# Kernel optimization log

Measured on AMD Instinct MI355X. Metric: run time of the kernel, lower is better.

## Reference

```python
import jax, jax.numpy as jnp
import numpy as np

NH, HS, K = 32, 2048, 16
HD = HS // NH
B, L = 4, 2048
EPS = 1e-6

def _ln(x, gamma, beta):
    mu = x.mean(-1, keepdims=True)
    var = x.var(-1, keepdims=True)  # ddof=0 == torch unbiased=False
    return gamma * ((x - mu) / jnp.sqrt(var + EPS)) + beta

def _ln_fused_l2_bwd(x, target, gamma, beta):
    D = x.shape[-1]
    mu = x.mean(-1, keepdims=True)
    std = jnp.sqrt(x.var(-1, keepdims=True) + EPS)
    xh = (x - mu) / std
    gxh = (gamma * xh + beta - target) * gamma
    return (D * gxh - gxh.sum(-1, keepdims=True) - xh * (gxh * xh).sum(-1, keepdims=True)) / (D * std)

def setup_inputs() -> dict:
    key = jax.random.key(0)
    ks = jax.random.split(key, 8)
    s = 0.02
    return {
        'hidden_states': jax.random.normal(ks[0], (B, L, HS), jnp.float32),
        'position_ids': jnp.tile(jnp.arange(L, dtype=jnp.int32)[None], (B, 1)),
        'q_w': jax.random.normal(ks[1], (HS, HS), jnp.float32) * s,
        'k_w': jax.random.normal(ks[2], (HS, HS), jnp.float32) * s,
        'v_w': jax.random.normal(ks[3], (HS, HS), jnp.float32) * s,
        'o_w': jax.random.normal(ks[4], (HS, HS), jnp.float32) * s,
        'W1': jax.random.normal(ks[5], (NH, HD, HD), jnp.float32) * s,
        'b1': jnp.zeros((NH, 1, HD), jnp.float32),
        'ttt_norm_weight': jnp.ones((NH, HD), jnp.float32),
        'ttt_norm_bias': jnp.zeros((NH, HD), jnp.float32),
        'ttt_lr_weight': jax.random.normal(ks[6], (NH, 1, HS), jnp.float32) * s,
        'ttt_lr_bias': jnp.zeros((NH, 1), jnp.float32),
        'learnable_token_idx': jnp.zeros((K,), jnp.float32),
        'post_norm_weight': jnp.ones((HS,), jnp.float32),
        'post_norm_bias': jnp.zeros((HS,), jnp.float32),
    }

def _forward(hidden_states, q_w, k_w, v_w, o_w, W1, b1, ttt_norm_weight,
             ttt_norm_bias, ttt_lr_weight, ttt_lr_bias, learnable_token_idx,
             post_norm_weight, post_norm_bias):
    Bb, Ll, _ = hidden_states.shape
    NM = Ll // K

    def proj_heads(w):
        return (hidden_states @ w.T).reshape(Bb, Ll, NH, HD).transpose(0, 2, 1, 3)

    XQ = proj_heads(q_w).reshape(Bb, NH, NM, K, HD)
    XK = proj_heads(k_w).reshape(Bb, NH, NM, K, HD)
    XV = proj_heads(v_w).reshape(Bb, NH, NM, K, HD)
    X = hidden_states.reshape(Bb, NM, K, HS)

    # eta: learned per-token lr gate, [B,nh,NM,K,K]
    ttt_lr = jnp.einsum('bnkc,hdc->bhnkd', X, ttt_lr_weight) + ttt_lr_bias.reshape(1, NH, 1, 1, 1)
    ttt_lr_eta = jax.nn.sigmoid(ttt_lr).transpose(0, 1, 2, 4, 3) / HD  # ttt_base_lr = 1.0
    token_idx = jnp.clip(1.0 / jnp.arange(1, K + 1, dtype=jnp.float32) + learnable_token_idx, 0.0, None)
    eta = token_idx.reshape(1, 1, 1, K, 1) * ttt_lr_eta

    ln_w = ttt_norm_weight.reshape(NH, 1, HD)
    ln_b = ttt_norm_bias.reshape(NH, 1, HD)

    def step(carry, x):
        W1_s, b1_s = carry                 # [B,nh,hd,hd], [B,nh,1,hd]
        xq, xk, xv, eta_mb = x             # [B,nh,K,hd], eta_mb [B,nh,K,K]
        Z1 = xk @ W1_s + b1_s
        grad = _ln_fused_l2_bwd(Z1, xv - xk, ln_w, ln_b)
        Attn1 = jnp.tril(xq @ xk.swapaxes(-1, -2))
        b1_bar = b1_s - jnp.tril(eta_mb) @ grad
        Z1_bar = xq @ W1_s - (eta_mb * Attn1) @ grad + b1_bar
        last_eta = eta_mb[:, :, -1, :, None]  # [B,nh,K,1]
        W1_new = W1_s - (last_eta * xk).swapaxes(-1, -2) @ grad
        b1_new = b1_s - jnp.sum(last_eta * grad, axis=-2, keepdims=True)
        out = xq + _ln(Z1_bar, ln_w, ln_b)
        return (W1_new, b1_new), out

    init = (jnp.tile(W1[None], (Bb, 1, 1, 1)), jnp.tile(b1[None], (Bb, 1, 1, 1)))
    xs = (XQ.transpose(2, 0, 1, 3, 4), XK.transpose(2, 0, 1, 3, 4),
          XV.transpose(2, 0, 1, 3, 4), eta.transpose(2, 0, 1, 3, 4))
    _, ys = jax.lax.scan(step, init, xs)          # [NM,B,nh,K,hd]
    out = ys.transpose(1, 0, 3, 2, 4).reshape(Bb, Ll, HS)
    out = _ln(out, post_norm_weight, post_norm_bias)  # post_norm (eps 1e-6)
    return out @ o_w.T

def reference(hidden_states, position_ids, q_w, k_w, v_w, o_w, W1, b1,
              ttt_norm_weight, ttt_norm_bias, ttt_lr_weight, ttt_lr_bias,
              learnable_token_idx, post_norm_weight, post_norm_bias):
    del position_ids  # unused in the shown forward (rope never applied)
    return _forward(hidden_states, q_w, k_w, v_w, o_w, W1, b1, ttt_norm_weight,
                    ttt_norm_bias, ttt_lr_weight, ttt_lr_bias, learnable_token_idx,
                    post_norm_weight, post_norm_bias)
```

## Files before the change

kernel.cpp:

```cpp
#include <hip/hip_runtime.h>

typedef unsigned short u16;
typedef unsigned int u32;
typedef __bf16 bf16_t;
typedef bf16_t bf16x8 __attribute__((ext_vector_type(8)));
typedef float f32x4 __attribute__((ext_vector_type(4)));
typedef u16 u16x8 __attribute__((ext_vector_type(8)));

#define B_   4
#define L_   2048
#define HS_  2048
#define NH_  32
#define HD_  64
#define KK_  16
#define NM_  128
#define M_   (B_*L_)

__device__ __forceinline__ u16 f2bf(float f) {
  unsigned u = __float_as_uint(f);
  u += 0x7FFFu + ((u >> 16) & 1u);
  return (u16)(u >> 16);
}
__device__ __forceinline__ float bf2f(u16 u) {
  return __uint_as_float(((unsigned)u) << 16);
}
__device__ __forceinline__ f32x4 vshfl_xor(f32x4 v, int m) {
  f32x4 r;
  r[0] = __shfl_xor(v[0], m, 64); r[1] = __shfl_xor(v[1], m, 64);
  r[2] = __shfl_xor(v[2], m, 64); r[3] = __shfl_xor(v[3], m, 64);
  return r;
}

__global__ __launch_bounds__(256) void cast_f32_bf16(const float* __restrict__ in,
                                                     u16* __restrict__ out, int n) {
  int i = (blockIdx.x * 256 + threadIdx.x) * 8;
  if (i >= n) return;
  float4 a = *(const float4*)(in + i);
  float4 b = *(const float4*)(in + i + 4);
  u16x8 o;
  o[0]=f2bf(a.x); o[1]=f2bf(a.y); o[2]=f2bf(a.z); o[3]=f2bf(a.w);
  o[4]=f2bf(b.x); o[5]=f2bf(b.y); o[6]=f2bf(b.z); o[7]=f2bf(b.w);
  *(u16x8*)(out + i) = o;
}

#define BM 128
#define BN 128
#define BK 32
#define LDT 40

template <bool BF16OUT>
__global__ __launch_bounds__(256) void gemm_nt(const u16* __restrict__ A,
                                               const u16* __restrict__ Bt,
                                               void* __restrict__ Cv,
                                               int M, int N, int K) {
  __shared__ u16 As[BM * LDT];
  __shared__ u16 Bs[BN * LDT];
  int tid  = threadIdx.x;
  int lane = tid & 63, wave = tid >> 6;
  int quad = lane >> 4, l16 = lane & 15;
  int bM = blockIdx.x * BM, bN = blockIdx.y * BN;
  int wM = (wave >> 1) * 64, wN = (wave & 1) * 64;
  int r0 = tid >> 2, c0 = (tid & 3) * 8;
  const u16* Ap = A + (size_t)bM * K;
  const u16* Bp = Bt + (size_t)bN * K;
  f32x4 acc[4][4] = {};
  u16x8 pa0 = *(const u16x8*)(Ap + (size_t)r0 * K + c0);
  u16x8 pa1 = *(const u16x8*)(Ap + (size_t)(r0 + 64) * K + c0);
  u16x8 pb0 = *(const u16x8*)(Bp + (size_t)r0 * K + c0);
  u16x8 pb1 = *(const u16x8*)(Bp + (size_t)(r0 + 64) * K + c0);
  int nk = K / BK;
  for (int kt = 0; kt < nk; ++kt) {
    *(u16x8*)&As[r0 * LDT + c0]        = pa0;
    *(u16x8*)&As[(r0 + 64) * LDT + c0] = pa1;
    *(u16x8*)&Bs[r0 * LDT + c0]        = pb0;
    *(u16x8*)&Bs[(r0 + 64) * LDT + c0] = pb1;
    __syncthreads();
    if (kt + 1 < nk) {
      int k0 = (kt + 1) * BK + c0;
      pa0 = *(const u16x8*)(Ap + (size_t)r0 * K + k0);
      pa1 = *(const u16x8*)(Ap + (size_t)(r0 + 64) * K + k0);
      pb0 = *(const u16x8*)(Bp + (size_t)r0 * K + k0);
      pb1 = *(const u16x8*)(Bp + (size_t)(r0 + 64) * K + k0);
    }
    bf16x8 af[4], bfr[4];
#pragma unroll
    for (int i = 0; i < 4; ++i) {
      u16x8 t = *(const u16x8*)&As[(wM + i * 16 + l16) * LDT + quad * 8];
      af[i] = __builtin_bit_cast(bf16x8, t);
    }
#pragma unroll
    for (int j = 0; j < 4; ++j) {
      u16x8 t = *(const u16x8*)&Bs[(wN + j * 16 + l16) * LDT + quad * 8];
      bfr[j] = __builtin_bit_cast(bf16x8, t);
    }
#pragma unroll
    for (int i = 0; i < 4; ++i) {
#pragma unroll
      for (int j = 0; j < 4; ++j)
        acc[i][j] = __builtin_amdgcn_mfma_f32_16x16x32_bf16(af[i], bfr[j], acc[i][j], 0, 0, 0);
    }
    __syncthreads();
  }
#pragma unroll
  for (int i = 0; i < 4; ++i) {
#pragma unroll
    for (int j = 0; j < 4; ++j) {
      int row = bM + wM + i * 16 + quad * 4;
      int col = bN + wN + j * 16 + l16;
      if (BF16OUT) {
        u16* cp = (u16*)Cv + (size_t)row * N + col;
#pragma unroll
        for (int r = 0; r < 4; ++r) cp[(size_t)r * N] = f2bf(acc[i][j][r]);
      } else {
        float* cp = (float*)Cv + (size_t)row * N + col;
#pragma unroll
        for (int r = 0; r < 4; ++r) cp[(size_t)r * N] = acc[i][j][r];
      }
    }
  }
}

__global__ __launch_bounds__(256) void sig_kernel(const u16* __restrict__ hsb,
                                                  const u16* __restrict__ lrwb,
                                                  const float* __restrict__ lrb,
                                                  float* __restrict__ Sig) {
  __shared__ u16 Bs[32 * LDT];
  int tid = threadIdx.x;
  int lane = tid & 63, wave = tid >> 6;
  int quad = lane >> 4, l16 = lane & 15;
  int m0 = blockIdx.x * 64 + wave * 16;
  f32x4 acc0 = {}, acc1 = {};
  for (int kt = 0; kt < HS_ / BK; ++kt) {
    int k0 = kt * BK;
    if (tid < 128) {
      int r = tid >> 2, c8 = (tid & 3) * 8;
      *(u16x8*)&Bs[r * LDT + c8] = *(const u16x8*)(lrwb + (size_t)r * HS_ + k0 + c8);
    }
    __syncthreads();
    u16x8 ta = *(const u16x8*)(hsb + (size_t)(m0 + l16) * HS_ + k0 + quad * 8);
    u16x8 t0 = *(const u16x8*)&Bs[l16 * LDT + quad * 8];
    u16x8 t1 = *(const u16x8*)&Bs[(16 + l16) * LDT + quad * 8];
    bf16x8 af  = __builtin_bit_cast(bf16x8, ta);
    bf16x8 bf0 = __builtin_bit_cast(bf16x8, t0);
    bf16x8 bf1 = __builtin_bit_cast(bf16x8, t1);
    acc0 = __builtin_amdgcn_mfma_f32_16x16x32_bf16(af, bf0, acc0, 0, 0, 0);
    acc1 = __builtin_amdgcn_mfma_f32_16x16x32_bf16(af, bf1, acc1, 0, 0, 0);
    __syncthreads();
  }
#pragma unroll
  for (int j = 0; j < 2; ++j) {
    f32x4 a = j ? acc1 : acc0;
    int h = j * 16 + l16;
    float bias = lrb[h];
#pragma unroll
    for (int r = 0; r < 4; ++r) {
      int m = m0 + quad * 4 + r;
      float v = a[r] + bias;
      float s = (1.f / (1.f + expf(-v))) * (1.f / 64.f);
      Sig[(size_t)m * NH_ + h] = s;
    }
  }
}

__global__ __launch_bounds__(256) void ttt_scan_mfma(
    const u16* __restrict__ XQ, const u16* __restrict__ XK, const u16* __restrict__ XV,
    const float* __restrict__ Sig, const float* __restrict__ W1_0, const float* __restrict__ b1_0,
    const float* __restrict__ lnw, const float* __restrict__ lnb, const float* __restrict__ lti,
    float* __restrict__ Y) {
  __shared__ u16 xkq[32 * 72];
  __shared__ u16 W1t[64 * 72];
  __shared__ u16 gradT[64 * 40];
  __shared__ u16 coefA[16 * 40];
  __shared__ u16 xkT[64 * 40];
  __shared__ float diff[16 * 68];
  __shared__ float red1[128], red2[128], red3[128];
  __shared__ float sig_s[16];

  int tid = threadIdx.x, wave = tid >> 6, lane = tid & 63;
  int quad = lane >> 4, l16 = lane & 15;
  int bh = blockIdx.x, b = bh >> 5, h = bh & 31;
  int dcol = wave * 16 + l16;

  {
    u32* p = (u32*)gradT; for (int i = tid; i < 1280; i += 256) p[i] = 0;
    u32* q = (u32*)coefA; for (int i = tid; i < 320;  i += 256) q[i] = 0;
    u32* s = (u32*)xkT;   for (int i = tid; i < 1280; i += 256) s[i] = 0;
  }

  f32x4 master[4];
  const float* wsrc = W1_0 + (size_t)h * 4096 + (size_t)dcol * 64;
#pragma unroll
  for (int m = 0; m < 4; ++m)
#pragma unroll
    for (int r = 0; r < 4; ++r) master[m][r] = wsrc[m * 16 + quad * 4 + r];
#pragma unroll
  for (int m = 0; m < 4; ++m)
#pragma unroll
    for (int r = 0; r < 4; ++r)
      W1t[(m * 16 + quad * 4 + r) * 72 + dcol] = f2bf(master[m][r]);

  float b1_reg = b1_0[h * 64 + dcol];
  float gamma_r = lnw[h * 64 + dcol], beta_r = lnb[h * 64 + dcol];
  f32x4 tok4;
#pragma unroll
  for (int r = 0; r < 4; ++r) {
    int kk = quad * 4 + r;
    tok4[r] = fmaxf(1.0f / (float)(kk + 1) + lti[kk], 0.0f);
  }
  float tok15 = fmaxf(1.0f / 16.0f + lti[15], 0.0f);

  int lrow = (tid < 128) ? (tid >> 3) : ((tid - 128) >> 3);
  int lc8  = (tid & 7) * 8;
  size_t rowstep = (size_t)HS_;
  size_t gb0 = ((size_t)(b * L_ + lrow)) * HS_ + h * HD_ + lc8;

  u16x8 rq, rv, rk;
  float rsig = 0.f;
  {
    size_t g = gb0;
    if (tid < 128) { rq = *(const u16x8*)(XQ + g); rv = *(const u16x8*)(XV + g); rk = *(const u16x8*)(XK + g); }
    else           { rk = *(const u16x8*)(XK + g); }
    if (tid < 16) rsig = Sig[(size_t)(b * L_ + tid) * NH_ + h];
  }
  __syncthreads();

  for (int n = 0; n < NM_; ++n) {
    if (tid < 128) {
      *(u16x8*)&xkq[(16 + lrow) * 72 + lc8] = rq;
      float4 d0, d1;
      d0.x = bf2f(rv[0]) - bf2f(rk[0]); d0.y = bf2f(rv[1]) - bf2f(rk[1]);
      d0.z = bf2f(rv[2]) - bf2f(rk[2]); d0.w = bf2f(rv[3]) - bf2f(rk[3]);
      d1.x = bf2f(rv[4]) - bf2f(rk[4]); d1.y = bf2f(rv[5]) - bf2f(rk[5]);
      d1.z = bf2f(rv[6]) - bf2f(rk[6]); d1.w = bf2f(rv[7]) - bf2f(rk[7]);
      *(float4*)&diff[lrow * 68 + lc8]     = d0;
      *(float4*)&diff[lrow * 68 + lc8 + 4] = d1;
    } else {
      *(u16x8*)&xkq[lrow * 72 + lc8] = rk;
#pragma unroll
      for (int i = 0; i < 8; ++i)
        xkT[(lc8 + i) * 40 + lrow] = f2bf(-tok15 * bf2f(rk[i]));
    }
    if (tid < 16) sig_s[tid] = rsig;
    __syncthreads();

    if (n + 1 < NM_) {
      size_t g = gb0 + (size_t)(n + 1) * KK_ * rowstep;
      if (tid < 128) { rq = *(const u16x8*)(XQ + g); rv = *(const u16x8*)(XV + g); rk = *(const u16x8*)(XK + g); }
      else           { rk = *(const u16x8*)(XK + g); }
      if (tid < 16) rsig = Sig[(size_t)(b * L_ + (n + 1) * KK_ + tid) * NH_ + h];
    }

    bf16x8 fxk[2], fxq[2], fw[2];
#pragma unroll
    for (int kc = 0; kc < 2; ++kc) {
      fxk[kc] = __builtin_bit_cast(bf16x8, *(const u16x8*)&xkq[l16 * 72 + kc * 32 + quad * 8]);
      fxq[kc] = __builtin_bit_cast(bf16x8, *(const u16x8*)&xkq[(16 + l16) * 72 + kc * 32 + quad * 8]);
      fw[kc]  = __builtin_bit_cast(bf16x8, *(const u16x8*)&W1t[(wave * 16 + l16) * 72 + kc * 32 + quad * 8]);
    }
    f32x4 z1 = {}, zq = {};
#pragma unroll
    for (int kc = 0; kc < 2; ++kc) {
      z1 = __builtin_amdgcn_mfma_f32_16x16x32_bf16(fxk[kc], fw[kc], z1, 0, 0, 0);
      zq = __builtin_amdgcn_mfma_f32_16x16x32_bf16(fxq[kc], fw[kc], zq, 0, 0, 0);
    }
    if (wave == 0) {
      f32x4 at = {};
#pragma unroll
      for (int kc = 0; kc < 2; ++kc)
        at = __builtin_amdgcn_mfma_f32_16x16x32_bf16(fxq[kc], fxk[kc], at, 0, 0, 0);
#pragma unroll
      for (int r = 0; r < 4; ++r) {
        int kk = quad * 4 + r;
        float c = (l16 <= kk) ? tok4[r] * (1.0f + at[r]) : 0.0f;
        coefA[kk * 40 + l16] = f2bf(-c);
      }
    }
#pragma unroll
    for (int r = 0; r < 4; ++r) z1[r] += b1_reg;

    {
      f32x4 s1 = z1, s2 = z1 * z1;
#pragma unroll
      for (int m = 1; m <= 8; m <<= 1) { s1 = s1 + vshfl_xor(s1, m); s2 = s2 + vshfl_xor(s2, m); }
      if (l16 == 0) {
#pragma unroll
        for (int r = 0; r < 4; ++r) {
          red1[quad * 32 + r * 8 + wave]     = s1[r];
          red1[quad * 32 + r * 8 + 4 + wave] = s2[r];
        }
      }
    }
    __syncthreads();
    f32x4 mu, rstd;
#pragma unroll
    for (int r = 0; r < 4; ++r) {
      f32x4 a = *(const f32x4*)&red1[quad * 32 + r * 8];
      f32x4 c = *(const f32x4*)&red1[quad * 32 + r * 8 + 4];
      float S = a[0] + a[1] + a[2] + a[3];
      float SS = c[0] + c[1] + c[2] + c[3];
      mu[r] = S * (1.0f / 64.0f);
      float var = SS * (1.0f / 64.0f) - mu[r] * mu[r];
      rstd[r] = 1.0f / sqrtf(var + 1e-6f);
    }
    f32x4 xh, gxh;
#pragma unroll
    for (int r = 0; r < 4; ++r) {
      float dd = diff[(quad * 4 + r) * 68 + dcol];
      xh[r] = (z1[r] - mu[r]) * rstd[r];
      gxh[r] = (gamma_r * xh[r] + beta_r - dd) * gamma_r;
    }
    {
      f32x4 s1 = gxh, s2 = gxh * xh;
#pragma unroll
      for (int m = 1; m <= 8; m <<= 1) { s1 = s1 + vshfl_xor(s1, m); s2 = s2 + vshfl_xor(s2, m); }
      if (l16 == 0) {
#pragma unroll
        for (int r = 0; r < 4; ++r) {
          red2[quad * 32 + r * 8 + wave]     = s1[r];
          red2[quad * 32 + r * 8 + 4 + wave] = s2[r];
        }
      }
    }
    __syncthreads();
    f32x4 grad;
#pragma unroll
    for (int r = 0; r < 4; ++r) {
      f32x4 a = *(const f32x4*)&red2[quad * 32 + r * 8];
      f32x4 c = *(const f32x4*)&red2[quad * 32 + r * 8 + 4];
      float S1v = a[0] + a[1] + a[2] + a[3];
      float S2v = c[0] + c[1] + c[2] + c[3];
      grad[r] = (64.0f * gxh[r] - S1v - xh[r] * S2v) * (rstd[r] * (1.0f / 64.0f));
    }
#pragma unroll
    for (int r = 0; r < 4; ++r) {
      float sk = sig_s[quad * 4 + r];
      gradT[dcol * 40 + quad * 4 + r] = f2bf(sk * grad[r]);
    }
    __syncthreads();

    bf16x8 fA = __builtin_bit_cast(bf16x8, *(const u16x8*)&coefA[l16 * 40 + quad * 8]);
    bf16x8 fG = __builtin_bit_cast(bf16x8, *(const u16x8*)&gradT[(wave * 16 + l16) * 40 + quad * 8]);
    f32x4 zb = __builtin_amdgcn_mfma_f32_16x16x32_bf16(fA, fG, zq, 0, 0, 0);
#pragma unroll
    for (int r = 0; r < 4; ++r) zb[r] += b1_reg;
    {
      bf16x8 fX = __builtin_bit_cast(bf16x8, *(const u16x8*)&xkT[(wave * 16 + l16) * 40 + quad * 8]);
#pragma unroll
      for (int m = 0; m < 4; ++m) {
        bf16x8 fGm = __builtin_bit_cast(bf16x8, *(const u16x8*)&gradT[(m * 16 + l16) * 40 + quad * 8]);
        master[m] = __builtin_amdgcn_mfma_f32_16x16x32_bf16(fGm, fX, master[m], 0, 0, 0);
      }
      float bs = 0.f;
#pragma unroll
      for (int j = 0; j < 8; ++j) bs += (float)fG[j];
      bs += __shfl_xor(bs, 16, 64);
      bs += __shfl_xor(bs, 32, 64);
      b1_reg -= tok15 * bs;
    }
    {
      f32x4 s1 = zb, s2 = zb * zb;
#pragma unroll
      for (int m = 1; m <= 8; m <<= 1) { s1 = s1 + vshfl_xor(s1, m); s2 = s2 + vshfl_xor(s2, m); }
      if (l16 == 0) {
#pragma unroll
        for (int r = 0; r < 4; ++r) {
          red3[quad * 32 + r * 8 + wave]     = s1[r];
          red3[quad * 32 + r * 8 + 4 + wave] = s2[r];
        }
      }
    }
    __syncthreads();
#pragma unroll
    for (int r = 0; r < 4; ++r) {
      f32x4 a = *(const f32x4*)&red3[quad * 32 + r * 8];
      f32x4 c = *(const f32x4*)&red3[quad * 32 + r * 8 + 4];
      float S = a[0] + a[1] + a[2] + a[3];
      float SS = c[0] + c[1] + c[2] + c[3];
      float mu2 = S * (1.0f / 64.0f);
      float var2 = SS * (1.0f / 64.0f) - mu2 * mu2;
      float rstd2 = 1.0f / sqrtf(var2 + 1e-6f);
      float xq_pass = bf2f(xkq[(16 + quad * 4 + r) * 72 + dcol]);
      float yv = xq_pass + gamma_r * ((zb[r] - mu2) * rstd2) + beta_r;
      Y[((size_t)(b * L_ + n * KK_ + quad * 4 + r)) * HS_ + h * HD_ + dcol] = yv;
    }
#pragma unroll
    for (int m = 0; m < 4; ++m)
#pragma unroll
      for (int r = 0; r < 4; ++r)
        W1t[(m * 16 + quad * 4 + r) * 72 + dcol] = f2bf(master[m][r]);
    __syncthreads();
  }
}

__global__ __launch_bounds__(256) void postnorm(const float* __restrict__ Yin,
                                                const float* __restrict__ w,
                                                const float* __restrict__ bb,
                                                u16* __restrict__ Yn) {
  __shared__ float red[8];
  int row = blockIdx.x, tid = threadIdx.x;
  const float* x = Yin + (size_t)row * HS_ + tid * 8;
  float4 v0 = *(const float4*)(x);
  float4 v1 = *(const float4*)(x + 4);
  float s  = v0.x + v0.y + v0.z + v0.w + v1.x + v1.y + v1.z + v1.w;
  float ss = v0.x*v0.x + v0.y*v0.y + v0.z*v0.z + v0.w*v0.w
           + v1.x*v1.x + v1.y*v1.y + v1.z*v1.z + v1.w*v1.w;
#pragma unroll
  for (int m = 32; m > 0; m >>= 1) { s += __shfl_xor(s, m, 64); ss += __shfl_xor(ss, m, 64); }
  int wave = tid >> 6, lane = tid & 63;
  if (lane == 0) { red[wave] = s; red[4 + wave] = ss; }
  __syncthreads();
  float S  = red[0] + red[1] + red[2] + red[3];
  float SS = red[4] + red[5] + red[6] + red[7];
  float mu = S * (1.f / 2048.f);
  float var = SS * (1.f / 2048.f) - mu * mu;
  float rstd = 1.f / sqrtf(var + 1e-6f);
  const float* wp = w + tid * 8;
  const float* bp = bb + tid * 8;
  float vals[8] = {v0.x, v0.y, v0.z, v0.w, v1.x, v1.y, v1.z, v1.w};
  u16x8 o;
#pragma unroll
  for (int t = 0; t < 8; ++t) o[t] = f2bf(wp[t] * ((vals[t] - mu) * rstd) + bp[t]);
  *(u16x8*)(Yn + (size_t)row * HS_ + tid * 8) = o;
}

extern "C" void kernel_launch(void* const* d_in, const int* in_sizes, int n_in,
                              void* d_out, int out_size, void* d_ws, size_t ws_size,
                              hipStream_t stream) {
  (void)in_sizes; (void)n_in; (void)out_size; (void)ws_size;
  const float* hidden = (const float*)d_in[0];
  const float* q_w = (const float*)d_in[2];
  const float* k_w = (const float*)d_in[3];
  const float* v_w = (const float*)d_in[4];
  const float* o_w = (const float*)d_in[5];
  const float* W1  = (const float*)d_in[6];
  const float* b1i = (const float*)d_in[7];
  const float* lnw = (const float*)d_in[8];
  const float* lnb = (const float*)d_in[9];
  const float* lrw = (const float*)d_in[10];
  const float* lrb = (const float*)d_in[11];
  const float* lti = (const float*)d_in[12];
  const float* pnw = (const float*)d_in[13];
  const float* pnb = (const float*)d_in[14];
  float* out = (float*)d_out;

  char* w = (char*)d_ws;
  u16* hsb  = (u16*)w;  w += (size_t)16777216 * 2;
  u16* wb   = (u16*)w;  w += (size_t)4194304 * 2;
  u16* lrwb = (u16*)w;  w += (size_t)65536 * 2;
  u16* XQb  = (u16*)w;  w += (size_t)16777216 * 2;
  u16* XKb  = (u16*)w;  w += (size_t)16777216 * 2;
  u16* XVb  = (u16*)w;  w += (size_t)16777216 * 2;
  float* Sg = (float*)w; w += (size_t)M_ * NH_ * 4;
  u16* Yn = hsb;

  cast_f32_bf16<<<8192, 256, 0, stream>>>(hidden, hsb, 16777216);
  cast_f32_bf16<<<32, 256, 0, stream>>>(lrw, lrwb, 65536);

  sig_kernel<<<128, 256, 0, stream>>>(hsb, lrwb, lrb, Sg);

  dim3 gg(M_ / BM, HS_ / BN);
  cast_f32_bf16<<<2048, 256, 0, stream>>>(q_w, wb, 4194304);
  gemm_nt<true><<<gg, 256, 0, stream>>>(hsb, wb, XQb, M_, HS_, HS_);
  cast_f32_bf16<<<2048, 256, 0, stream>>>(k_w, wb, 4194304);
  gemm_nt<true><<<gg, 256, 0, stream>>>(hsb, wb, XKb, M_, HS_, HS_);
  cast_f32_bf16<<<2048, 256, 0, stream>>>(v_w, wb, 4194304);
  gemm_nt<true><<<gg, 256, 0, stream>>>(hsb, wb, XVb, M_, HS_, HS_);

  ttt_scan_mfma<<<128, 256, 0, stream>>>(XQb, XKb, XVb, Sg, W1, b1i, lnw, lnb, lti, out);

  postnorm<<<8192, 256, 0, stream>>>(out, pnw, pnb, Yn);

  cast_f32_bf16<<<2048, 256, 0, stream>>>(o_w, wb, 4194304);
  gemm_nt<false><<<gg, 256, 0, stream>>>(Yn, wb, out, M_, HS_, HS_);
}
```

Baseline: 1.017 ms.

## Run TTT scan with one wave per head, removing block barriers

```diff
diff --git a/kernel.cpp b/kernel.cpp
--- a/kernel.cpp
+++ b/kernel.cpp
@@ -162,45 +162,55 @@
   }
 }
 
-__global__ __launch_bounds__(256) void ttt_scan_mfma(
+__global__ __launch_bounds__(64, 1) void ttt_scan_wave(
     const u16* __restrict__ XQ, const u16* __restrict__ XK, const u16* __restrict__ XV,
     const float* __restrict__ Sig, const float* __restrict__ W1_0, const float* __restrict__ b1_0,
     const float* __restrict__ lnw, const float* __restrict__ lnb, const float* __restrict__ lti,
     float* __restrict__ Y) {
-  __shared__ u16 xkq[32 * 72];
   __shared__ u16 W1t[64 * 72];
   __shared__ u16 gradT[64 * 40];
   __shared__ u16 coefA[16 * 40];
   __shared__ u16 xkT[64 * 40];
-  __shared__ float diff[16 * 68];
-  __shared__ float red1[128], red2[128], red3[128];
-  __shared__ float sig_s[16];
-
-  int tid = threadIdx.x, wave = tid >> 6, lane = tid & 63;
+  __shared__ float diffS[16 * 68];
+  __shared__ float xqF[16 * 68];
+
+  int lane = threadIdx.x;
   int quad = lane >> 4, l16 = lane & 15;
   int bh = blockIdx.x, b = bh >> 5, h = bh & 31;
-  int dcol = wave * 16 + l16;
 
   {
-    u32* p = (u32*)gradT; for (int i = tid; i < 1280; i += 256) p[i] = 0;
-    u32* q = (u32*)coefA; for (int i = tid; i < 320;  i += 256) q[i] = 0;
-    u32* s = (u32*)xkT;   for (int i = tid; i < 1280; i += 256) s[i] = 0;
-  }
-
-  f32x4 master[4];
-  const float* wsrc = W1_0 + (size_t)h * 4096 + (size_t)dcol * 64;
-#pragma unroll
-  for (int m = 0; m < 4; ++m)
-#pragma unroll
-    for (int r = 0; r < 4; ++r) master[m][r] = wsrc[m * 16 + quad * 4 + r];
-#pragma unroll
-  for (int m = 0; m < 4; ++m)
-#pragma unroll
-    for (int r = 0; r < 4; ++r)
-      W1t[(m * 16 + quad * 4 + r) * 72 + dcol] = f2bf(master[m][r]);
-
-  float b1_reg = b1_0[h * 64 + dcol];
-  float gamma_r = lnw[h * 64 + dcol], beta_r = lnb[h * 64 + dcol];
+    u32* p = (u32*)gradT; for (int i = lane; i < 1280; i += 64) p[i] = 0;
+    u32* q = (u32*)coefA; for (int i = lane; i < 320;  i += 64) q[i] = 0;
+    u32* s = (u32*)xkT;   for (int i = lane; i < 1280; i += 64) s[i] = 0;
+  }
+
+  f32x4 master[4][4];
+  {
+    const float* wsrc = W1_0 + (size_t)h * 4096;
+#pragma unroll
+    for (int c = 0; c < 4; ++c) {
+      const float* wc = wsrc + (size_t)(c * 16 + l16) * 64 + quad * 4;
+#pragma unroll
+      for (int a = 0; a < 4; ++a)
+#pragma unroll
+        for (int r = 0; r < 4; ++r) master[a][c][r] = wc[a * 16 + r];
+    }
+  }
+#pragma unroll
+  for (int a = 0; a < 4; ++a)
+#pragma unroll
+    for (int c = 0; c < 4; ++c)
+#pragma unroll
+      for (int r = 0; r < 4; ++r)
+        W1t[(a * 16 + quad * 4 + r) * 72 + c * 16 + l16] = f2bf(master[a][c][r]);
+
+  f32x4 b1r, gam, bet;
+#pragma unroll
+  for (int c = 0; c < 4; ++c) {
+    b1r[c] = b1_0[h * 64 + c * 16 + l16];
+    gam[c] = lnw[h * 64 + c * 16 + l16];
+    bet[c] = lnb[h * 64 + c * 16 + l16];
+  }
   f32x4 tok4;
 #pragma unroll
   for (int r = 0; r < 4; ++r) {
@@ -209,186 +219,192 @@
   }
   float tok15 = fmaxf(1.0f / 16.0f + lti[15], 0.0f);
 
-  int lrow = (tid < 128) ? (tid >> 3) : ((tid - 128) >> 3);
-  int lc8  = (tid & 7) * 8;
-  size_t rowstep = (size_t)HS_;
-  size_t gb0 = ((size_t)(b * L_ + lrow)) * HS_ + h * HD_ + lc8;
-
-  u16x8 rq, rv, rk;
-  float rsig = 0.f;
-  {
-    size_t g = gb0;
-    if (tid < 128) { rq = *(const u16x8*)(XQ + g); rv = *(const u16x8*)(XV + g); rk = *(const u16x8*)(XK + g); }
-    else           { rk = *(const u16x8*)(XK + g); }
-    if (tid < 16) rsig = Sig[(size_t)(b * L_ + tid) * NH_ + h];
-  }
-  __syncthreads();
+  size_t gb  = ((size_t)(b * L_ + l16)) * HS_ + h * HD_ + quad * 8;
+  size_t sgb = (size_t)(b * L_ + l16) * NH_ + h;
+
+  u16x8 cxk[2], cxq[2], cxv[2];
+  float csig;
+#pragma unroll
+  for (int kc = 0; kc < 2; ++kc) {
+    cxk[kc] = *(const u16x8*)(XK + gb + kc * 32);
+    cxq[kc] = *(const u16x8*)(XQ + gb + kc * 32);
+    cxv[kc] = *(const u16x8*)(XV + gb + kc * 32);
+  }
+  csig = Sig[sgb];
 
   for (int n = 0; n < NM_; ++n) {
-    if (tid < 128) {
-      *(u16x8*)&xkq[(16 + lrow) * 72 + lc8] = rq;
-      float4 d0, d1;
-      d0.x = bf2f(rv[0]) - bf2f(rk[0]); d0.y = bf2f(rv[1]) - bf2f(rk[1]);
-      d0.z = bf2f(rv[2]) - bf2f(rk[2]); d0.w = bf2f(rv[3]) - bf2f(rk[3]);
-      d1.x = bf2f(rv[4]) - bf2f(rk[4]); d1.y = bf2f(rv[5]) - bf2f(rk[5]);
-      d1.z = bf2f(rv[6]) - bf2f(rk[6]); d1.w = bf2f(rv[7]) - bf2f(rk[7]);
-      *(float4*)&diff[lrow * 68 + lc8]     = d0;
-      *(float4*)&diff[lrow * 68 + lc8 + 4] = d1;
-    } else {
-      *(u16x8*)&xkq[lrow * 72 + lc8] = rk;
-#pragma unroll
-      for (int i = 0; i < 8; ++i)
-        xkT[(lc8 + i) * 40 + lrow] = f2bf(-tok15 * bf2f(rk[i]));
-    }
-    if (tid < 16) sig_s[tid] = rsig;
-    __syncthreads();
+    bf16x8 fw[4][2];
+#pragma unroll
+    for (int cb = 0; cb < 4; ++cb)
+#pragma unroll
+      for (int kc = 0; kc < 2; ++kc)
+        fw[cb][kc] = __builtin_bit_cast(bf16x8,
+            *(const u16x8*)&W1t[(cb * 16 + l16) * 72 + kc * 32 + quad * 8]);
+
+#pragma unroll
+    for (int kc = 0; kc < 2; ++kc) {
+      float dv[8], qv[8];
+#pragma unroll
+      for (int j = 0; j < 8; ++j) {
+        dv[j] = bf2f(cxv[kc][j]) - bf2f(cxk[kc][j]);
+        qv[j] = bf2f(cxq[kc][j]);
+      }
+      float4 d0 = {dv[0], dv[1], dv[2], dv[3]}, d1 = {dv[4], dv[5], dv[6], dv[7]};
+      float4 q0 = {qv[0], qv[1], qv[2], qv[3]}, q1 = {qv[4], qv[5], qv[6], qv[7]};
+      *(float4*)&diffS[l16 * 68 + kc * 32 + quad * 8]     = d0;
+      *(float4*)&diffS[l16 * 68 + kc * 32 + quad * 8 + 4] = d1;
+      *(float4*)&xqF[l16 * 68 + kc * 32 + quad * 8]       = q0;
+      *(float4*)&xqF[l16 * 68 + kc * 32 + quad * 8 + 4]   = q1;
+#pragma unroll
+      for (int j = 0; j < 8; ++j)
+        xkT[(kc * 32 + quad * 8 + j) * 40 + l16] = f2bf(-tok15 * bf2f(cxk[kc][j]));
+    }
+    f32x4 ssig;
+#pragma unroll
+    for (int r = 0; r < 4; ++r) ssig[r] = __shfl(csig, quad * 4 + r, 64);
+
+    bf16x8 fxk[2], fxq[2];
+#pragma unroll
+    for (int kc = 0; kc < 2; ++kc) {
+      fxk[kc] = __builtin_bit_cast(bf16x8, cxk[kc]);
+      fxq[kc] = __builtin_bit_cast(bf16x8, cxq[kc]);
+    }
 
     if (n + 1 < NM_) {
-      size_t g = gb0 + (size_t)(n + 1) * KK_ * rowstep;
-      if (tid < 128) { rq = *(const u16x8*)(XQ + g); rv = *(const u16x8*)(XV + g); rk = *(const u16x8*)(XK + g); }
-      else           { rk = *(const u16x8*)(XK + g); }
-      if (tid < 16) rsig = Sig[(size_t)(b * L_ + (n + 1) * KK_ + tid) * NH_ + h];
-    }
-
-    bf16x8 fxk[2], fxq[2], fw[2];
+      size_t g = gb + (size_t)(n + 1) * KK_ * HS_;
+#pragma unroll
+      for (int kc = 0; kc < 2; ++kc) {
+        cxk[kc] = *(const u16x8*)(XK + g + kc * 32);
+        cxq[kc] = *(const u16x8*)(XQ + g + kc * 32);
+        cxv[kc] = *(const u16x8*)(XV + g + kc * 32);
+      }
+      csig = Sig[sgb + (size_t)(n + 1) * KK_ * NH_];
+    }
+
+    f32x4 z1[4] = {}, zq[4] = {}, at = {};
 #pragma unroll
     for (int kc = 0; kc < 2; ++kc) {
-      fxk[kc] = __builtin_bit_cast(bf16x8, *(const u16x8*)&xkq[l16 * 72 + kc * 32 + quad * 8]);
-      fxq[kc] = __builtin_bit_cast(bf16x8, *(const u16x8*)&xkq[(16 + l16) * 72 + kc * 32 + quad * 8]);
-      fw[kc]  = __builtin_bit_cast(bf16x8, *(const u16x8*)&W1t[(wave * 16 + l16) * 72 + kc * 32 + quad * 8]);
-    }
-    f32x4 z1 = {}, zq = {};
-#pragma unroll
-    for (int kc = 0; kc < 2; ++kc) {
-      z1 = __builtin_amdgcn_mfma_f32_16x16x32_bf16(fxk[kc], fw[kc], z1, 0, 0, 0);
-      zq = __builtin_amdgcn_mfma_f32_16x16x32_bf16(fxq[kc], fw[kc], zq, 0, 0, 0);
-    }
-    if (wave == 0) {
-      f32x4 at = {};
-#pragma unroll
-      for (int kc = 0; kc < 2; ++kc)
-        at = __builtin_amdgcn_mfma_f32_16x16x32_bf16(fxq[kc], fxk[kc], at, 0, 0, 0);
+      at = __builtin_amdgcn_mfma_f32_16x16x32_bf16(fxq[kc], fxk[kc], at, 0, 0, 0);
+#pragma unroll
+      for (int cb = 0; cb < 4; ++cb) {
+        z1[cb] = __builtin_amdgcn_mfma_f32_16x16x32_bf16(fxk[kc], fw[cb][kc], z1[cb], 0, 0, 0);
+        zq[cb] = __builtin_amdgcn_mfma_f32_16x16x32_bf16(fxq[kc], fw[cb][kc], zq[cb], 0, 0, 0);
+      }
+    }
+
+#pragma unroll
+    for (int r = 0; r < 4; ++r) {
+      int kk = quad * 4 + r;
+      float cc = (l16 <= kk) ? tok4[r] * (1.0f + at[r]) : 0.0f;
+      coefA[kk * 40 + l16] = f2bf(-cc);
+    }
+
+    f32x4 dd[4], xqr[4];
+#pragma unroll
+    for (int cb = 0; cb < 4; ++cb)
 #pragma unroll
       for (int r = 0; r < 4; ++r) {
-        int kk = quad * 4 + r;
-        float c = (l16 <= kk) ? tok4[r] * (1.0f + at[r]) : 0.0f;
-        coefA[kk * 40 + l16] = f2bf(-c);
-      }
-    }
-#pragma unroll
-    for (int r = 0; r < 4; ++r) z1[r] += b1_reg;
-
-    {
-      f32x4 s1 = z1, s2 = z1 * z1;
-#pragma unroll
-      for (int m = 1; m <= 8; m <<= 1) { s1 = s1 + vshfl_xor(s1, m); s2 = s2 + vshfl_xor(s2, m); }
-      if (l16 == 0) {
-#pragma unroll
-        for (int r = 0; r < 4; ++r) {
-          red1[quad * 32 + r * 8 + wave]     = s1[r];
-          red1[quad * 32 + r * 8 + 4 + wave] = s2[r];
-        }
-      }
-    }
-    __syncthreads();
+        dd[cb][r]  = diffS[(quad * 4 + r) * 68 + cb * 16 + l16];
+        xqr[cb][r] = xqF[(quad * 4 + r) * 68 + cb * 16 + l16];
+      }
+
+    f32x4 s1 = {}, s2 = {};
+#pragma unroll
+    for (int cb = 0; cb < 4; ++cb) {
+#pragma unroll
+      for (int r = 0; r < 4; ++r) z1[cb][r] += b1r[cb];
+      s1 = s1 + z1[cb];
+      s2 = s2 + z1[cb] * z1[cb];
+    }
+#pragma unroll
+    for (int m = 1; m <= 8; m <<= 1) { s1 = s1 + vshfl_xor(s1, m); s2 = s2 + vshfl_xor(s2, m); }
     f32x4 mu, rstd;
 #pragma unroll
     for (int r = 0; r < 4; ++r) {
-      f32x4 a = *(const f32x4*)&red1[quad * 32 + r * 8];
-      f32x4 c = *(const f32x4*)&red1[quad * 32 + r * 8 + 4];
-      float S = a[0] + a[1] + a[2] + a[3];
-      float SS = c[0] + c[1] + c[2] + c[3];
-      mu[r] = S * (1.0f / 64.0f);
-      float var = SS * (1.0f / 64.0f) - mu[r] * mu[r];
+      mu[r] = s1[r] * (1.0f / 64.0f);
+      float var = s2[r] * (1.0f / 64.0f) - mu[r] * mu[r];
       rstd[r] = 1.0f / sqrtf(var + 1e-6f);
     }
-    f32x4 xh, gxh;
+
+    f32x4 xh[4], gxh[4], t1v = {}, t2v = {};
+#pragma unroll
+    for (int cb = 0; cb < 4; ++cb) {
+#pragma unroll
+      for (int r = 0; r < 4; ++r) {
+        xh[cb][r]  = (z1[cb][r] - mu[r]) * rstd[r];
+        gxh[cb][r] = (gam[cb] * xh[cb][r] + bet[cb] - dd[cb][r]) * gam[cb];
+      }
+      t1v = t1v + gxh[cb];
+      t2v = t2v + gxh[cb] * xh[cb];
+    }
+#pragma unroll
+    for (int m = 1; m <= 8; m <<= 1) { t1v = t1v + vshfl_xor(t1v, m); t2v = t2v + vshfl_xor(t2v, m); }
+
+    f32x4 bsum = {};
+#pragma unroll
+    for (int cb = 0; cb < 4; ++cb) {
+      float sg[4];
+#pragma unroll
+      for (int r = 0; r < 4; ++r) {
+        float g = (64.0f * gxh[cb][r] - t1v[r] - xh[cb][r] * t2v[r]) * (rstd[r] * (1.0f / 64.0f));
+        sg[r] = ssig[r] * g;
+      }
+      u32 p0 = (u32)f2bf(sg[0]) | ((u32)f2bf(sg[1]) << 16);
+      u32 p1 = (u32)f2bf(sg[2]) | ((u32)f2bf(sg[3]) << 16);
+      *(u32*)&gradT[(cb * 16 + l16) * 40 + quad * 4]     = p0;
+      *(u32*)&gradT[(cb * 16 + l16) * 40 + quad * 4 + 2] = p1;
+      bsum[cb] = sg[0] + sg[1] + sg[2] + sg[3];
+    }
+    bsum = bsum + vshfl_xor(bsum, 16);
+    bsum = bsum + vshfl_xor(bsum, 32);
+
+    bf16x8 fA = __builtin_bit_cast(bf16x8, *(const u16x8*)&coefA[l16 * 40 + quad * 8]);
+    bf16x8 fG[4], fX[4];
+#pragma unroll
+    for (int cb = 0; cb < 4; ++cb) {
+      fG[cb] = __builtin_bit_cast(bf16x8, *(const u16x8*)&gradT[(cb * 16 + l16) * 40 + quad * 8]);
+      fX[cb] = __builtin_bit_cast(bf16x8, *(const u16x8*)&xkT[(cb * 16 + l16) * 40 + quad * 8]);
+    }
+
+    f32x4 zb[4];
+#pragma unroll
+    for (int cb = 0; cb < 4; ++cb) {
+      zb[cb] = __builtin_amdgcn_mfma_f32_16x16x32_bf16(fA, fG[cb], zq[cb], 0, 0, 0);
+#pragma unroll
+      for (int r = 0; r < 4; ++r) zb[cb][r] += b1r[cb];
+    }
+
+#pragma unroll
+    for (int a = 0; a < 4; ++a)
+#pragma unroll
+      for (int c = 0; c < 4; ++c)
+        master[a][c] = __builtin_amdgcn_mfma_f32_16x16x32_bf16(fG[a], fX[c], master[a][c], 0, 0, 0);
+#pragma unroll
+    for (int c = 0; c < 4; ++c) b1r[c] -= tok15 * bsum[c];
+
+    f32x4 w1s = {}, w2s = {};
+#pragma unroll
+    for (int cb = 0; cb < 4; ++cb) { w1s = w1s + zb[cb]; w2s = w2s + zb[cb] * zb[cb]; }
+#pragma unroll
+    for (int m = 1; m <= 8; m <<= 1) { w1s = w1s + vshfl_xor(w1s, m); w2s = w2s + vshfl_xor(w2s, m); }
 #pragma unroll
     for (int r = 0; r < 4; ++r) {
-      float dd = diff[(quad * 4 + r) * 68 + dcol];
-      xh[r] = (z1[r] - mu[r]) * rstd[r];
-      gxh[r] = (gamma_r * xh[r] + beta_r - dd) * gamma_r;
-    }
-    {
-      f32x4 s1 = gxh, s2 = gxh * xh;
-#pragma unroll
-      for (int m = 1; m <= 8; m <<= 1) { s1 = s1 + vshfl_xor(s1, m); s2 = s2 + vshfl_xor(s2, m); }
-      if (l16 == 0) {
-#pragma unroll
-        for (int r = 0; r < 4; ++r) {
-          red2[quad * 32 + r * 8 + wave]     = s1[r];
-          red2[quad * 32 + r * 8 + 4 + wave] = s2[r];
-        }
-      }
-    }
-    __syncthreads();
-    f32x4 grad;
-#pragma unroll
-    for (int r = 0; r < 4; ++r) {
-      f32x4 a = *(const f32x4*)&red2[quad * 32 + r * 8];
-      f32x4 c = *(const f32x4*)&red2[quad * 32 + r * 8 + 4];
-      float S1v = a[0] + a[1] + a[2] + a[3];
-      float S2v = c[0] + c[1] + c[2] + c[3];
-      grad[r] = (64.0f * gxh[r] - S1v - xh[r] * S2v) * (rstd[r] * (1.0f / 64.0f));
-    }
-#pragma unroll
-    for (int r = 0; r < 4; ++r) {
-      float sk = sig_s[quad * 4 + r];
-      gradT[dcol * 40 + quad * 4 + r] = f2bf(sk * grad[r]);
-    }
-    __syncthreads();
-
-    bf16x8 fA = __builtin_bit_cast(bf16x8, *(const u16x8*)&coefA[l16 * 40 + quad * 8]);
-    bf16x8 fG = __builtin_bit_cast(bf16x8, *(const u16x8*)&gradT[(wave * 16 + l16) * 40 + quad * 8]);
-    f32x4 zb = __builtin_amdgcn_mfma_f32_16x16x32_bf16(fA, fG, zq, 0, 0, 0);
-#pragma unroll
-    for (int r = 0; r < 4; ++r) zb[r] += b1_reg;
-    {
-      bf16x8 fX = __builtin_bit_cast(bf16x8, *(const u16x8*)&xkT[(wave * 16 + l16) * 40 + quad * 8]);
-#pragma unroll
-      for (int m = 0; m < 4; ++m) {
-        bf16x8 fGm = __builtin_bit_cast(bf16x8, *(const u16x8*)&gradT[(m * 16 + l16) * 40 + quad * 8]);
-        master[m] = __builtin_amdgcn_mfma_f32_16x16x32_bf16(fGm, fX, master[m], 0, 0, 0);
-      }
-      float bs = 0.f;
-#pragma unroll
-      for (int j = 0; j < 8; ++j) bs += (float)fG[j];
-      bs += __shfl_xor(bs, 16, 64);
-      bs += __shfl_xor(bs, 32, 64);
-      b1_reg -= tok15 * bs;
-    }
-    {
-      f32x4 s1 = zb, s2 = zb * zb;
-#pragma unroll
-      for (int m = 1; m <= 8; m <<= 1) { s1 = s1 + vshfl_xor(s1, m); s2 = s2 + vshfl_xor(s2, m); }
-      if (l16 == 0) {
-#pragma unroll
-        for (int r = 0; r < 4; ++r) {
-          red3[quad * 32 + r * 8 + wave]     = s1[r];
-          red3[quad * 32 + r * 8 + 4 + wave] = s2[r];
-        }
-      }
-    }
-    __syncthreads();
-#pragma unroll
-    for (int r = 0; r < 4; ++r) {
-      f32x4 a = *(const f32x4*)&red3[quad * 32 + r * 8];
-      f32x4 c = *(const f32x4*)&red3[quad * 32 + r * 8 + 4];
-      float S = a[0] + a[1] + a[2] + a[3];
-      float SS = c[0] + c[1] + c[2] + c[3];
-      float mu2 = S * (1.0f / 64.0f);
-      float var2 = SS * (1.0f / 64.0f) - mu2 * mu2;
+      float mu2 = w1s[r] * (1.0f / 64.0f);
+      float var2 = w2s[r] * (1.0f / 64.0f) - mu2 * mu2;
       float rstd2 = 1.0f / sqrtf(var2 + 1e-6f);
-      float xq_pass = bf2f(xkq[(16 + quad * 4 + r) * 72 + dcol]);
-      float yv = xq_pass + gamma_r * ((zb[r] - mu2) * rstd2) + beta_r;
-      Y[((size_t)(b * L_ + n * KK_ + quad * 4 + r)) * HS_ + h * HD_ + dcol] = yv;
-    }
-#pragma unroll
-    for (int m = 0; m < 4; ++m)
-#pragma unroll
-      for (int r = 0; r < 4; ++r)
-        W1t[(m * 16 + quad * 4 + r) * 72 + dcol] = f2bf(master[m][r]);
-    __syncthreads();
+      float* yp = Y + ((size_t)(b * L_ + n * KK_ + quad * 4 + r)) * HS_ + h * HD_ + l16;
+#pragma unroll
+      for (int cb = 0; cb < 4; ++cb)
+        yp[cb * 16] = xqr[cb][r] + gam[cb] * ((zb[cb][r] - mu2) * rstd2) + bet[cb];
+    }
+
+#pragma unroll
+    for (int a = 0; a < 4; ++a)
+#pragma unroll
+      for (int c = 0; c < 4; ++c)
+#pragma unroll
+        for (int r = 0; r < 4; ++r)
+          W1t[(a * 16 + quad * 4 + r) * 72 + c * 16 + l16] = f2bf(master[a][c][r]);
   }
 }
 
@@ -466,7 +482,7 @@
   cast_f32_bf16<<<2048, 256, 0, stream>>>(v_w, wb, 4194304);
   gemm_nt<true><<<gg, 256, 0, stream>>>(hsb, wb, XVb, M_, HS_, HS_);
 
-  ttt_scan_mfma<<<128, 256, 0, stream>>>(XQb, XKb, XVb, Sg, W1, b1i, lnw, lnb, lti, out);
+  ttt_scan_wave<<<128, 64, 0, stream>>>(XQb, XKb, XVb, Sg, W1, b1i, lnw, lnb, lti, out);
 
   postnorm<<<8192, 256, 0, stream>>>(out, pnw, pnb, Yn);
 
```

Result: slower. 1.053 ms (+3.5%).
